# Optimization experiments

Hardware: AMD Instinct MI355X
Metric: run time of the kernel (lower is better)

The kernel has to match this reference:

```python
import jax, jax.numpy as jnp
import numpy as np

NUM_HEADS = 12


def setup_inputs() -> dict:
    key = jax.random.key(0)
    k1, k2, k3, k4, k5 = jax.random.split(key, 5)
    B, N, C = 4, 1024, 768
    x = jax.random.normal(k1, (B, N, C), dtype=jnp.float32)
    y = jax.random.normal(k2, (B, N, C), dtype=jnp.float32)
    w_qkv = jax.random.normal(k3, (4 * C, C), dtype=jnp.float32) * 0.02
    w_proj = jax.random.normal(k4, (C, C), dtype=jnp.float32) * 0.02
    b_proj = jax.random.normal(k5, (C,), dtype=jnp.float32) * 0.02
    return {"x": x, "y": y, "w_qkv": w_qkv, "w_proj": w_proj, "b_proj": b_proj}


def reference(x, y, w_qkv, w_proj, b_proj):
    B, N, C = x.shape
    H = NUM_HEADS
    hd = C // H
    scale = hd ** (-0.5)

    def qkv4(t):
        # Linear(dim, 4*dim, bias=False): t @ W^T -> [B,N,4C] -> [4,B,H,N,hd]
        p = (t @ w_qkv.T).reshape(B, N, 4, H, hd).transpose(2, 0, 3, 1, 4)
        return p[0], p[1], p[2], p[3]

    qxo, qx, kx, vx = qkv4(x)
    qyo, qy, ky, _vy_from_y = qkv4(y)
    vy = vx  # faithful to source: vy = qkv[3] (from x), not qkv2[3]

    def attend(q, k, v, neg):
        s = jnp.einsum('bhnd,bhmd->bhnm', q, k) * scale
        a = jax.nn.softmax(-s if neg else s, axis=-1)
        o = jnp.einsum('bhnm,bhmd->bhnd', a, v)
        return o.transpose(0, 2, 1, 3).reshape(B, N, C)

    x_self = attend(qx, kx, vx, False)
    y_self = attend(qy, ky, vy, False)
    x_cross = attend(qyo, kx, vx, True)   # attnx = -(qyo @ kx^T)
    y_cross = attend(qxo, ky, vy, True)   # attny = -(qxo @ ky^T)

    out_x = (x_self + x_cross) @ w_proj.T + b_proj
    out_y = (y_self + y_cross) @ w_proj.T + b_proj
    return (out_x, out_y)
```

## Files before the change

kernel.cpp:

```cpp
#include <hip/hip_runtime.h>
#include <hip/hip_bf16.h>
#include <stdint.h>


#define BB 4
#define NN 1024
#define CC 768
#define HH 12
#define HD 64

typedef unsigned short u16;
typedef short short8 __attribute__((ext_vector_type(8)));
typedef float f32x4 __attribute__((ext_vector_type(4)));

extern "C" __device__ float __ocml_native_exp2_f32(float);

__device__ __forceinline__ u16 f2bf(float f) {
  unsigned int u = __float_as_uint(f);
  return (u16)((u + 0x7fffu + ((u >> 16) & 1u)) >> 16);
}

__device__ __forceinline__ void load_lds16(const u16* g, u16* l) {
  __builtin_amdgcn_global_load_lds((__attribute__((address_space(1))) const void*)g,
                                   (__attribute__((address_space(3))) void*)l, 16, 0, 0);
}

__global__ __launch_bounds__(256)
void cvt_bf16(const float* __restrict__ x, const float* __restrict__ y,
              const float* __restrict__ wq, const float* __restrict__ wp,
              u16* __restrict__ xb, u16* __restrict__ yb,
              u16* __restrict__ wqb, u16* __restrict__ wpb)
{
  const int seg = blockIdx.y;
  const float* src = seg == 0 ? x : (seg == 1 ? y : (seg == 2 ? wq : wp));
  u16* dst = seg == 0 ? xb : (seg == 1 ? yb : (seg == 2 ? wqb : wpb));
  const int n = (seg == 3) ? 768 * 768 : ((seg == 2) ? 3072 * 768 : 4096 * 768);
  const int i = (blockIdx.x * 256 + threadIdx.x) * 8;
  if (i >= n) return;
  float sc = 1.0f;
  if (seg == 2) {
    const int row = i / 768;
    sc = (row < 768) ? -0.18033688f : (row < 1536 ? 0.18033688f : 1.0f);
  }
  float4 a = *(const float4*)(src + i);
  float4 b = *(const float4*)(src + i + 4);
  ushort4 u0 = {f2bf(a.x * sc), f2bf(a.y * sc), f2bf(a.z * sc), f2bf(a.w * sc)};
  ushort4 u1 = {f2bf(b.x * sc), f2bf(b.y * sc), f2bf(b.z * sc), f2bf(b.w * sc)};
  *(ushort4*)(dst + i) = u0;
  *(ushort4*)(dst + i + 4) = u1;
}

__global__ __launch_bounds__(256)
void vtrans(const u16* __restrict__ qkvx, u16* __restrict__ VT)
{
  const int bh = blockIdx.y, b = bh / HH, h = bh % HH;
  const int t = threadIdx.x;
  const int key = blockIdx.x * 32 + (t >> 3), d0 = (t & 7) * 8;
  uint4 v = *(const uint4*)(qkvx + (size_t)(b * NN + key) * 3072 + 3 * CC + h * HD + d0);
  u16 e[8];
  *(uint4*)e = v;
#pragma unroll
  for (int i = 0; i < 8; i++)
    VT[(size_t)(bh * 64 + d0 + i) * 1024 + key] = e[i];
}

template<int NP, bool BF16OUT, bool BIAS>
__global__ __launch_bounds__(256)
void gemm_mfma(const u16* __restrict__ A0, const u16* __restrict__ A1,
               const u16* __restrict__ W, const float* __restrict__ bias,
               void* __restrict__ C0, void* __restrict__ C1)
{
  __shared__ u16 As[128 * 64];
  __shared__ u16 Bs[128 * 64];
  const u16* A = blockIdx.z ? A1 : A0;
  void* C = blockIdx.z ? C1 : C0;
  const int m0 = blockIdx.y * 128, n0 = blockIdx.x * 128;
  const int t = threadIdx.x, w = t >> 6, lane = t & 63;
  const int c = lane & 15, qq = lane >> 4;
  const int mq = (w >> 1) * 64, nq = (w & 1) * 64;

  const int lrow = lane >> 3;
  const int lchunk = (lane & 7) ^ lrow;
  size_t arow[4], brow[4];
#pragma unroll
  for (int i = 0; i < 4; i++) {
    const int r = (w * 4 + i) * 8 + lrow;
    arow[i] = (size_t)(m0 + r) * 768 + lchunk * 8;
    brow[i] = (size_t)(n0 + r) * 768 + lchunk * 8;
  }

  f32x4 acc[4][4] = {};
  for (int k0 = 0; k0 < 768; k0 += 64) {
    __syncthreads();
#pragma unroll
    for (int i = 0; i < 4; i++) {
      load_lds16(A + arow[i] + k0, As + (w * 4 + i) * 512);
      load_lds16(W + brow[i] + k0, Bs + (w * 4 + i) * 512);
    }
    __syncthreads();
#pragma unroll
    for (int s = 0; s < 2; s++) {
      const int swz = ((s * 4 + qq) ^ (c & 7)) * 8;
      short8 af[4], bf[4];
#pragma unroll
      for (int i = 0; i < 4; i++)
        af[i] = *(const short8*)&As[(mq + i * 16 + c) * 64 + swz];
#pragma unroll
      for (int j = 0; j < 4; j++)
        bf[j] = *(const short8*)&Bs[(nq + j * 16 + c) * 64 + swz];
#pragma unroll
      for (int i = 0; i < 4; i++)
#pragma unroll
        for (int j = 0; j < 4; j++)
          acc[i][j] = __builtin_amdgcn_mfma_f32_16x16x32_bf16(af[i], bf[j], acc[i][j], 0, 0, 0);
    }
  }
  float bj[4] = {0.f, 0.f, 0.f, 0.f};
  if (BIAS) {
#pragma unroll
    for (int j = 0; j < 4; j++) bj[j] = bias[n0 + nq + c + j * 16];
  }
#pragma unroll
  for (int i = 0; i < 4; i++)
#pragma unroll
    for (int r = 0; r < 4; r++) {
      const size_t row = (size_t)(m0 + mq + i * 16 + qq * 4 + r) * NP + n0 + nq + c;
      if (BF16OUT) {
#pragma unroll
        for (int j = 0; j < 4; j++)
          ((u16*)C)[row + j * 16] = f2bf(acc[i][j][r]);
      } else {
#pragma unroll
        for (int j = 0; j < 4; j++)
          ((float*)C)[row + j * 16] = acc[i][j][r] + bj[j];
      }
    }
}

__global__ __launch_bounds__(256, 3)
void attn_pair_mfma(const u16* __restrict__ qkvx, const u16* __restrict__ qkvy,
                    const u16* __restrict__ VT,
                    u16* __restrict__ sum_x, u16* __restrict__ sum_y)
{
  __shared__ __align__(16) u16 smem[24576];
  float (*Of)[68] = (float(*)[68])smem;

  const int qt = blockIdx.x, bh = blockIdx.y, pair = blockIdx.z;
  const int b = bh / HH, head = bh % HH;
  const u16* q1 = pair ? qkvy : qkvx;
  const u16* q2 = pair ? qkvx : qkvy;
  const u16* ks = pair ? qkvy : qkvx;
  u16* outp = pair ? sum_y : sum_x;

  const int t = threadIdx.x, w = t >> 6, lane = t & 63;
  const int c = lane & 15, qq = lane >> 4;

  short8 Qf[4][2];
#pragma unroll
  for (int g = 0; g < 2; g++) {
    const int qrow = qt * 128 + g * 64 + w * 16 + c;
    const u16* qs = q1 + (size_t)(b * NN + qrow) * 3072 + CC + head * HD + qq * 8;
    const u16* qc = q2 + (size_t)(b * NN + qrow) * 3072 + head * HD + qq * 8;
    Qf[g * 2][0] = *(const short8*)qs;
    Qf[g * 2][1] = *(const short8*)(qs + 32);
    Qf[g * 2 + 1][0] = *(const short8*)qc;
    Qf[g * 2 + 1][1] = *(const short8*)(qc + 32);
  }

  const u16* kbase = ks + (size_t)(b * NN) * 3072 + 2 * CC + head * HD;
  const u16* vtb = VT + (size_t)(bh * 64) * 1024;

  const int lr = lane >> 3;
  const int sc8 = ((lane & 7) ^ lr) * 8;

  u16* Pw = smem + 8192 + w * 4096;

  short8 ones;
#pragma unroll
  for (int i = 0; i < 8; i++) ones[i] = (short)0x3F80;

  f32x4 O[4][4] = {};
  f32x4 L[4] = {};

  const int cx = c & 7;
  const int off0 = (qq ^ cx) * 8;
  const int off1 = ((4 + qq) ^ cx) * 8;

  for (int c16 = 0; c16 < 16; ++c16) {
    __syncthreads();
#pragma unroll
    for (int i = 0; i < 2; i++) {
      const int r = (2 * w + i) * 8 + lr;
      load_lds16(kbase + (size_t)(c16 * 64 + r) * 3072 + sc8,
                 smem + (2 * w + i) * 512);
      load_lds16(vtb + (size_t)r * 1024 + c16 * 64 + sc8,
                 smem + 4096 + (2 * w + i) * 512);
    }
    __syncthreads();

#pragma unroll
    for (int g = 0; g < 2; g++) {
      f32x4 ss[4], sx[4];
#pragma unroll
      for (int t4 = 0; t4 < 4; t4++) {
        const u16* kr = smem + (16 * t4 + c) * 64;
        short8 k0 = *(const short8*)(kr + off0);
        short8 k1 = *(const short8*)(kr + off1);
        f32x4 z = {0.f, 0.f, 0.f, 0.f};
        z = __builtin_amdgcn_mfma_f32_16x16x32_bf16(Qf[g * 2][0], k0, z, 0, 0, 0);
        ss[t4] = __builtin_amdgcn_mfma_f32_16x16x32_bf16(Qf[g * 2][1], k1, ss[t4] = z, 0, 0, 0);
        f32x4 z2 = {0.f, 0.f, 0.f, 0.f};
        z2 = __builtin_amdgcn_mfma_f32_16x16x32_bf16(Qf[g * 2 + 1][0], k0, z2, 0, 0, 0);
        sx[t4] = __builtin_amdgcn_mfma_f32_16x16x32_bf16(Qf[g * 2 + 1][1], k1, z2, 0, 0, 0);
      }
      u16* Ps = Pw + (g * 2) * 1024;
      u16* Pc = Ps + 1024;
#pragma unroll
      for (int t4 = 0; t4 < 4; t4++)
#pragma unroll
        for (int r = 0; r < 4; r++) {
          const int row = 4 * qq + r;
          const int poff = row * 64 + ((2 * t4 + (c >> 3)) ^ (row & 7)) * 8 + cx;
          float es = __ocml_native_exp2_f32(ss[t4][r]);
          float ec = __ocml_native_exp2_f32(sx[t4][r]);
          Ps[poff] = (u16)(__float_as_uint(es) >> 16);
          Pc[poff] = (u16)(__float_as_uint(ec) >> 16);
        }
    }

    short8 Pf[4][2];
#pragma unroll
    for (int s = 0; s < 4; s++) {
      const u16* pr = Pw + s * 1024 + c * 64;
      Pf[s][0] = *(const short8*)(pr + off0);
      Pf[s][1] = *(const short8*)(pr + off1);
      L[s] = __builtin_amdgcn_mfma_f32_16x16x32_bf16(Pf[s][0], ones, L[s], 0, 0, 0);
      L[s] = __builtin_amdgcn_mfma_f32_16x16x32_bf16(Pf[s][1], ones, L[s], 0, 0, 0);
    }
#pragma unroll
    for (int t4 = 0; t4 < 4; t4++) {
      const u16* vr = smem + 4096 + (16 * t4 + c) * 64;
      short8 v0 = *(const short8*)(vr + off0);
      short8 v1 = *(const short8*)(vr + off1);
#pragma unroll
      for (int s = 0; s < 4; s++) {
        O[s][t4] = __builtin_amdgcn_mfma_f32_16x16x32_bf16(Pf[s][0], v0, O[s][t4], 0, 0, 0);
        O[s][t4] = __builtin_amdgcn_mfma_f32_16x16x32_bf16(Pf[s][1], v1, O[s][t4], 0, 0, 0);
      }
    }
  }

  __syncthreads();
#pragma unroll
  for (int g = 0; g < 2; g++) {
    float is[4], ic[4];
#pragma unroll
    for (int r = 0; r < 4; r++) {
      is[r] = 1.0f / L[g * 2][r];
      ic[r] = 1.0f / L[g * 2 + 1][r];
    }
#pragma unroll
    for (int t4 = 0; t4 < 4; t4++)
#pragma unroll
      for (int r = 0; r < 4; r++)
        Of[g * 64 + w * 16 + 4 * qq + r][16 * t4 + c] =
            O[g * 2][t4][r] * is[r] + O[g * 2 + 1][t4][r] * ic[r];
  }
  __syncthreads();
#pragma unroll
  for (int p = 0; p < 8; p++) {
    const int idx = p * 256 + t;
    const int row = idx >> 4, c4 = (idx & 15) * 4;
    float4 v = *(const float4*)&Of[row][c4];
    ushort4 u = {f2bf(v.x), f2bf(v.y), f2bf(v.z), f2bf(v.w)};
    *(ushort4*)(outp + (size_t)(b * NN + qt * 128 + row) * CC + head * HD + c4) = u;
  }
}

extern "C" void kernel_launch(void* const* d_in, const int* in_sizes, int n_in,
                              void* d_out, int out_size, void* d_ws, size_t ws_size,
                              hipStream_t stream)
{
  const float* x      = (const float*)d_in[0];
  const float* y      = (const float*)d_in[1];
  const float* w_qkv  = (const float*)d_in[2];
  const float* w_proj = (const float*)d_in[3];
  const float* b_proj = (const float*)d_in[4];

  u16* qkv_x = (u16*)d_ws;
  u16* qkv_y = qkv_x + (size_t)4096 * 3072;
  u16* rest = qkv_y + (size_t)4096 * 3072;
  u16* sum_x = rest;
  u16* sum_y = sum_x + (size_t)4096 * 768;
  u16* x_bf  = rest;
  u16* y_bf  = x_bf + (size_t)4096 * 768;
  u16* wq_bf = y_bf + (size_t)4096 * 768;
  u16* wp_bf = wq_bf + (size_t)3072 * 768;
  u16* VT    = wp_bf + (size_t)768 * 768;
  float* out_x = (float*)d_out;
  float* out_y = out_x + (size_t)4096 * 768;

  cvt_bf16<<<dim3(1536, 4), 256, 0, stream>>>(x, y, w_qkv, w_proj,
                                              x_bf, y_bf, wq_bf, wp_bf);

  gemm_mfma<3072, true, false><<<dim3(24, 32, 2), 256, 0, stream>>>(
      x_bf, y_bf, wq_bf, nullptr, qkv_x, qkv_y);

  vtrans<<<dim3(32, 48), 256, 0, stream>>>(qkv_x, VT);

  attn_pair_mfma<<<dim3(8, 48, 2), 256, 0, stream>>>(qkv_x, qkv_y, VT, sum_x, sum_y);

  gemm_mfma<768, false, true><<<dim3(6, 32, 2), 256, 0, stream>>>(
      sum_x, sum_y, wp_bf, b_proj, out_x, out_y);
}
```

Measured before the change: 241.1 us.

## Double-buffer K/V tiles in attention and remap blocks per XCD

The attention kernel now double-buffers K and V^T tiles in LDS, issuing the next tile's async global-to-LDS loads before computing on the current one, which removes one barrier per iteration and overlaps memory with MFMA work. The P buffer per wave is shrunk and reused per query group, with the P·V MFMAs interleaved into the group loop. Both vtrans and attention switch to 1D grids whose block index is decoded so that blocks sharing a batch-head land on the same XCD, aiming for better L2 reuse of K/V. The risks are higher LDS and register pressure and the single barrier per iteration: the prefetch into the other buffer and this iteration's P buffer writes must not race with waves still reading them from the previous iteration.

```diff
diff --git a/kernel.cpp b/kernel.cpp
--- a/kernel.cpp
+++ b/kernel.cpp
@@ -53,9 +53,13 @@
 __global__ __launch_bounds__(256)
 void vtrans(const u16* __restrict__ qkvx, u16* __restrict__ VT)
 {
-  const int bh = blockIdx.y, b = bh / HH, h = bh % HH;
+  const int blk = blockIdx.x;
+  const int xcd = blk & 7, slot = blk >> 3;
+  const int bh = (slot >> 5) * 8 + xcd;
+  const int kt = slot & 31;
+  const int b = bh / HH, h = bh % HH;
   const int t = threadIdx.x;
-  const int key = blockIdx.x * 32 + (t >> 3), d0 = (t & 7) * 8;
+  const int key = kt * 32 + (t >> 3), d0 = (t & 7) * 8;
   uint4 v = *(const uint4*)(qkvx + (size_t)(b * NN + key) * 3072 + 3 * CC + h * HD + d0);
   u16 e[8];
   *(uint4*)e = v;
@@ -145,7 +149,10 @@
   __shared__ __align__(16) u16 smem[24576];
   float (*Of)[68] = (float(*)[68])smem;
 
-  const int qt = blockIdx.x, bh = blockIdx.y, pair = blockIdx.z;
+  const int blk = blockIdx.x;
+  const int xcd = blk & 7, slot = blk >> 3;
+  const int bh = (slot >> 4) * 8 + xcd;
+  const int qt = (slot & 15) >> 1, pair = slot & 1;
   const int b = bh / HH, head = bh % HH;
   const u16* q1 = pair ? qkvy : qkvx;
   const u16* q2 = pair ? qkvx : qkvy;
@@ -173,7 +180,7 @@
   const int lr = lane >> 3;
   const int sc8 = ((lane & 7) ^ lr) * 8;
 
-  u16* Pw = smem + 8192 + w * 4096;
+  u16* Pw = smem + 16384 + w * 2048;
 
   short8 ones;
 #pragma unroll
@@ -186,35 +193,42 @@
   const int off0 = (qq ^ cx) * 8;
   const int off1 = ((4 + qq) ^ cx) * 8;
 
-  for (int c16 = 0; c16 < 16; ++c16) {
-    __syncthreads();
+  auto stage = [&](int c16, int hf) {
+    const int bo = hf * 4096;
 #pragma unroll
     for (int i = 0; i < 2; i++) {
       const int r = (2 * w + i) * 8 + lr;
       load_lds16(kbase + (size_t)(c16 * 64 + r) * 3072 + sc8,
-                 smem + (2 * w + i) * 512);
+                 smem + bo + (2 * w + i) * 512);
       load_lds16(vtb + (size_t)r * 1024 + c16 * 64 + sc8,
-                 smem + 4096 + (2 * w + i) * 512);
-    }
+                 smem + 8192 + bo + (2 * w + i) * 512);
+    }
+  };
+
+  stage(0, 0);
+  for (int c16 = 0; c16 < 16; ++c16) {
     __syncthreads();
+    if (c16 < 15) stage(c16 + 1, (c16 + 1) & 1);
+    const u16* Kc = smem + (c16 & 1) * 4096;
+    const u16* Vc = smem + 8192 + (c16 & 1) * 4096;
 
 #pragma unroll
     for (int g = 0; g < 2; g++) {
       f32x4 ss[4], sx[4];
 #pragma unroll
       for (int t4 = 0; t4 < 4; t4++) {
-        const u16* kr = smem + (16 * t4 + c) * 64;
+        const u16* kr = Kc + (16 * t4 + c) * 64;
         short8 k0 = *(const short8*)(kr + off0);
         short8 k1 = *(const short8*)(kr + off1);
         f32x4 z = {0.f, 0.f, 0.f, 0.f};
         z = __builtin_amdgcn_mfma_f32_16x16x32_bf16(Qf[g * 2][0], k0, z, 0, 0, 0);
-        ss[t4] = __builtin_amdgcn_mfma_f32_16x16x32_bf16(Qf[g * 2][1], k1, ss[t4] = z, 0, 0, 0);
+        ss[t4] = __builtin_amdgcn_mfma_f32_16x16x32_bf16(Qf[g * 2][1], k1, z, 0, 0, 0);
         f32x4 z2 = {0.f, 0.f, 0.f, 0.f};
         z2 = __builtin_amdgcn_mfma_f32_16x16x32_bf16(Qf[g * 2 + 1][0], k0, z2, 0, 0, 0);
         sx[t4] = __builtin_amdgcn_mfma_f32_16x16x32_bf16(Qf[g * 2 + 1][1], k1, z2, 0, 0, 0);
       }
-      u16* Ps = Pw + (g * 2) * 1024;
-      u16* Pc = Ps + 1024;
+      u16* Ps = Pw;
+      u16* Pc2 = Pw + 1024;
 #pragma unroll
       for (int t4 = 0; t4 < 4; t4++)
 #pragma unroll
@@ -224,28 +238,28 @@
           float es = __ocml_native_exp2_f32(ss[t4][r]);
           float ec = __ocml_native_exp2_f32(sx[t4][r]);
           Ps[poff] = (u16)(__float_as_uint(es) >> 16);
-          Pc[poff] = (u16)(__float_as_uint(ec) >> 16);
+          Pc2[poff] = (u16)(__float_as_uint(ec) >> 16);
         }
-    }
-
-    short8 Pf[4][2];
-#pragma unroll
-    for (int s = 0; s < 4; s++) {
-      const u16* pr = Pw + s * 1024 + c * 64;
-      Pf[s][0] = *(const short8*)(pr + off0);
-      Pf[s][1] = *(const short8*)(pr + off1);
-      L[s] = __builtin_amdgcn_mfma_f32_16x16x32_bf16(Pf[s][0], ones, L[s], 0, 0, 0);
-      L[s] = __builtin_amdgcn_mfma_f32_16x16x32_bf16(Pf[s][1], ones, L[s], 0, 0, 0);
-    }
-#pragma unroll
-    for (int t4 = 0; t4 < 4; t4++) {
-      const u16* vr = smem + 4096 + (16 * t4 + c) * 64;
-      short8 v0 = *(const short8*)(vr + off0);
-      short8 v1 = *(const short8*)(vr + off1);
-#pragma unroll
-      for (int s = 0; s < 4; s++) {
-        O[s][t4] = __builtin_amdgcn_mfma_f32_16x16x32_bf16(Pf[s][0], v0, O[s][t4], 0, 0, 0);
-        O[s][t4] = __builtin_amdgcn_mfma_f32_16x16x32_bf16(Pf[s][1], v1, O[s][t4], 0, 0, 0);
+      short8 Pf[2][2];
+      const u16* prs = Ps + c * 64;
+      const u16* prc = Pc2 + c * 64;
+      Pf[0][0] = *(const short8*)(prs + off0);
+      Pf[0][1] = *(const short8*)(prs + off1);
+      Pf[1][0] = *(const short8*)(prc + off0);
+      Pf[1][1] = *(const short8*)(prc + off1);
+      L[g * 2] = __builtin_amdgcn_mfma_f32_16x16x32_bf16(Pf[0][0], ones, L[g * 2], 0, 0, 0);
+      L[g * 2] = __builtin_amdgcn_mfma_f32_16x16x32_bf16(Pf[0][1], ones, L[g * 2], 0, 0, 0);
+      L[g * 2 + 1] = __builtin_amdgcn_mfma_f32_16x16x32_bf16(Pf[1][0], ones, L[g * 2 + 1], 0, 0, 0);
+      L[g * 2 + 1] = __builtin_amdgcn_mfma_f32_16x16x32_bf16(Pf[1][1], ones, L[g * 2 + 1], 0, 0, 0);
+#pragma unroll
+      for (int t4 = 0; t4 < 4; t4++) {
+        const u16* vr = Vc + (16 * t4 + c) * 64;
+        short8 v0 = *(const short8*)(vr + off0);
+        short8 v1 = *(const short8*)(vr + off1);
+        O[g * 2][t4] = __builtin_amdgcn_mfma_f32_16x16x32_bf16(Pf[0][0], v0, O[g * 2][t4], 0, 0, 0);
+        O[g * 2][t4] = __builtin_amdgcn_mfma_f32_16x16x32_bf16(Pf[0][1], v1, O[g * 2][t4], 0, 0, 0);
+        O[g * 2 + 1][t4] = __builtin_amdgcn_mfma_f32_16x16x32_bf16(Pf[1][0], v0, O[g * 2 + 1][t4], 0, 0, 0);
+        O[g * 2 + 1][t4] = __builtin_amdgcn_mfma_f32_16x16x32_bf16(Pf[1][1], v1, O[g * 2 + 1][t4], 0, 0, 0);
       }
     }
   }
@@ -306,9 +320,9 @@
   gemm_mfma<3072, true, false><<<dim3(24, 32, 2), 256, 0, stream>>>(
       x_bf, y_bf, wq_bf, nullptr, qkv_x, qkv_y);
 
-  vtrans<<<dim3(32, 48), 256, 0, stream>>>(qkv_x, VT);
-
-  attn_pair_mfma<<<dim3(8, 48, 2), 256, 0, stream>>>(qkv_x, qkv_y, VT, sum_x, sum_y);
+  vtrans<<<dim3(1536), 256, 0, stream>>>(qkv_x, VT);
+
+  attn_pair_mfma<<<dim3(768), 256, 0, stream>>>(qkv_x, qkv_y, VT, sum_x, sum_y);
 
   gemm_mfma<768, false, true><<<dim3(6, 32, 2), 256, 0, stream>>>(
       sum_x, sum_y, wp_bf, b_proj, out_x, out_y);
```

Measured after the change: 245.4 us. No clear change (+1.8%).
